# Kernel optimization log

Measured on AMD Instinct MI355X. Metric: run time of the kernel, lower is better.

## Reference

```python
import jax, jax.numpy as jnp
import numpy as np

N = 100_000            # nodes
E = 1_600_000          # edges (avg degree 16)
IN, OUT = 64, 16
L1, L2 = 48, 32        # in - floor(k*(in-out)/3) for k=1,2
EDGE_DIM = 16
EPS = 1e-7             # GENConv message epsilon
BN_EPS = 1e-5


def _lin(k, i, o):
    return jax.random.normal(k, (i, o), jnp.float32) / np.float32(np.sqrt(i))


def setup_inputs() -> dict:
    key = jax.random.key(0)
    ks = jax.random.split(key, 16)
    z = lambda d: jnp.zeros((d,), jnp.float32)
    o = lambda d: jnp.ones((d,), jnp.float32)
    return {
        "x": jax.random.normal(ks[0], (N, IN), jnp.float32),
        "edge_index": jax.random.randint(ks[1], (2, E), 0, N),
        "edge_attr": jax.random.normal(ks[2], (E, EDGE_DIM), jnp.float32),
        # GENConv 1 (IN -> L1)
        "w_src1": _lin(ks[3], IN, L1), "b_src1": z(L1),
        "w_edge1": _lin(ks[4], EDGE_DIM, L1), "b_edge1": z(L1),
        "w_m1a": _lin(ks[5], L1, 2 * L1), "b_m1a": z(2 * L1),
        "g1": o(2 * L1), "be1": z(2 * L1),
        "w_m1b": _lin(ks[6], 2 * L1, L1), "b_m1b": z(L1),
        # GENConv 2 (L1 -> L2)
        "w_src2": _lin(ks[7], L1, L2), "b_src2": z(L2),
        "w_edge2": _lin(ks[8], EDGE_DIM, L2), "b_edge2": z(L2),
        "w_m2a": _lin(ks[9], L2, 2 * L2), "b_m2a": z(2 * L2),
        "g2": o(2 * L2), "be2": z(2 * L2),
        "w_m2b": _lin(ks[10], 2 * L2, L2), "b_m2b": z(L2),
        # GCNConv heads (L2 -> OUT)
        "w_mu": _lin(ks[11], L2, OUT), "b_mu": z(OUT),
        "w_ls": _lin(ks[12], L2, OUT), "b_ls": z(OUT),
    }


def _gen_conv(x, src, dst, e_raw, w_src, b_src, w_edge, b_edge,
              w1, b1, g, be, w2, b2):
    """PyG GENConv with softmax aggregation (t=1) and 2-layer MLP w/ batch norm."""
    h = x @ w_src + b_src                      # [N, d] lin_src
    e = e_raw @ w_edge + b_edge                # [E, d] lin_edge
    msg = jax.nn.relu(h[src] + e) + EPS        # [E, d] message
    # per-destination, per-channel softmax aggregation
    mmax = jax.ops.segment_max(msg, dst, num_segments=N)
    mmax = jnp.where(jnp.isfinite(mmax), mmax, 0.0)
    ex = jnp.exp(msg - mmax[dst])
    denom = jax.ops.segment_sum(ex, dst, num_segments=N)
    agg = jax.ops.segment_sum(ex * msg, dst, num_segments=N) / (denom + 1e-16)
    out = agg + h                              # residual with x_dst (lin_src applied)
    # MLP: Linear -> BatchNorm(train stats) -> ReLU -> Linear
    zt = out @ w1 + b1
    zt = (zt - zt.mean(0)) * jax.lax.rsqrt(zt.var(0) + BN_EPS) * g + be
    return jax.nn.relu(zt) @ w2 + b2


def _gcn_conv(x, src, dst, w, b):
    """PyG GCNConv: self-loops + symmetric normalization."""
    loop = jnp.arange(N)
    s = jnp.concatenate([src, loop])
    d = jnp.concatenate([dst, loop])
    deg = jax.ops.segment_sum(jnp.ones(s.shape, x.dtype), d, num_segments=N)
    dinv = jnp.where(deg > 0, jax.lax.rsqrt(deg), 0.0)
    norm = (dinv[s] * dinv[d])[:, None]
    return jax.ops.segment_sum((x @ w)[s] * norm, d, num_segments=N) + b


def reference(x, edge_index, edge_attr,
              w_src1, b_src1, w_edge1, b_edge1, w_m1a, b_m1a, g1, be1, w_m1b, b_m1b,
              w_src2, b_src2, w_edge2, b_edge2, w_m2a, b_m2a, g2, be2, w_m2b, b_m2b,
              w_mu, b_mu, w_ls, b_ls):
    src, dst = edge_index[0], edge_index[1]
    h = jax.nn.relu(_gen_conv(x, src, dst, edge_attr, w_src1, b_src1, w_edge1,
                              b_edge1, w_m1a, b_m1a, g1, be1, w_m1b, b_m1b))
    h = jax.nn.relu(_gen_conv(h, src, dst, edge_attr, w_src2, b_src2, w_edge2,
                              b_edge2, w_m2a, b_m2a, g2, be2, w_m2b, b_m2b))
    mu = _gcn_conv(h, src, dst, w_mu, b_mu)
    logstd = _gcn_conv(h, src, dst, w_ls, b_ls)
    return (mu, logstd)
```

## Files before the change

kernel.cpp:

```cpp
#include <hip/hip_runtime.h>
#include <hip/hip_bf16.h>

typedef unsigned int u32;

#define EPS_MSG 1e-7f
#define BN_EPS  1e-5f

template<int I, int O>
__global__ void k_lin(const float* __restrict__ X, const float* __restrict__ W,
                      const float* __restrict__ B, float* __restrict__ Y,
                      int ldY, int n) {
  __shared__ float Wl[I * O];
  __shared__ float Bl[O];
  for (int t = threadIdx.x; t < I * O; t += blockDim.x) Wl[t] = W[t];
  if (threadIdx.x < O) Bl[threadIdx.x] = B[threadIdx.x];
  __syncthreads();
  int i = blockIdx.x * blockDim.x + threadIdx.x;
  if (i >= n) return;
  float acc[O];
#pragma unroll
  for (int c = 0; c < O; c++) acc[c] = Bl[c];
  const float4* xp = (const float4*)(X + (size_t)i * I);
  for (int q = 0; q < I / 4; q++) {
    float4 v = xp[q];
#pragma unroll
    for (int c = 0; c < O; c++) acc[c] += v.x * Wl[(4 * q + 0) * O + c];
#pragma unroll
    for (int c = 0; c < O; c++) acc[c] += v.y * Wl[(4 * q + 1) * O + c];
#pragma unroll
    for (int c = 0; c < O; c++) acc[c] += v.z * Wl[(4 * q + 2) * O + c];
#pragma unroll
    for (int c = 0; c < O; c++) acc[c] += v.w * Wl[(4 * q + 3) * O + c];
  }
  float* y = Y + (size_t)i * ldY;
#pragma unroll
  for (int c = 0; c < O; c++) y[c] = acc[c];
}

__global__ void k_deg(const int* __restrict__ ei, u32* __restrict__ deg, int E) {
  int e = blockIdx.x * blockDim.x + threadIdx.x;
  if (e < E) atomicAdd(&deg[ei[E + e]], 1u);
}

__global__ void k_scan1(const u32* __restrict__ deg, u32* __restrict__ excl,
                        u32* __restrict__ part, int n) {
  __shared__ u32 sm[256];
  int t = threadIdx.x;
  int base = blockIdx.x * 1024 + t * 4;
  u32 v0 = (base + 0 < n) ? deg[base + 0] : 0u;
  u32 v1 = (base + 1 < n) ? deg[base + 1] : 0u;
  u32 v2 = (base + 2 < n) ? deg[base + 2] : 0u;
  u32 v3 = (base + 3 < n) ? deg[base + 3] : 0u;
  u32 tsum = v0 + v1 + v2 + v3;
  sm[t] = tsum;
  __syncthreads();
  for (int o = 1; o < 256; o <<= 1) {
    u32 v = (t >= o) ? sm[t - o] : 0u;
    __syncthreads();
    sm[t] += v;
    __syncthreads();
  }
  u32 tex = sm[t] - tsum;
  if (t == 255) part[blockIdx.x] = sm[255];
  if (base + 0 < n) excl[base + 0] = tex;
  if (base + 1 < n) excl[base + 1] = tex + v0;
  if (base + 2 < n) excl[base + 2] = tex + v0 + v1;
  if (base + 3 < n) excl[base + 3] = tex + v0 + v1 + v2;
}

__global__ void k_scan2(u32* __restrict__ part, int nb) {
  if (threadIdx.x == 0) {
    u32 acc = 0;
    for (int i = 0; i < nb; i++) { u32 v = part[i]; part[i] = acc; acc += v; }
  }
}

__global__ void k_scan3(u32* __restrict__ rowptr, const u32* __restrict__ part,
                        int n, int E) {
  int i = blockIdx.x * blockDim.x + threadIdx.x;
  if (i < n) rowptr[i] += part[i >> 10];
  if (i == 0) rowptr[n] = (u32)E;
}

template<bool PERM>
__global__ void k_slots(const int* __restrict__ ei, const u32* __restrict__ rowptr,
                        u32* __restrict__ cnt, int2* __restrict__ csr,
                        const float* __restrict__ ea, float* __restrict__ eaperm,
                        int E) {
  int e = blockIdx.x * blockDim.x + threadIdx.x;
  if (e >= E) return;
  int s = ei[e], d = ei[E + e];
  u32 slot = rowptr[d] + atomicAdd(&cnt[d], 1u);
  csr[slot] = make_int2(s, e);
  if (PERM) {
    const float4* p = (const float4*)(ea + (size_t)e * 16);
    float4* q = (float4*)(eaperm + (size_t)slot * 16);
    float4 a = p[0], b = p[1], c = p[2], dd = p[3];
    q[0] = a; q[1] = b; q[2] = c; q[3] = dd;
  }
}

__global__ void k_dinv(const u32* __restrict__ deg, float* __restrict__ dinv, int n) {
  int i = blockIdx.x * blockDim.x + threadIdx.x;
  if (i < n) dinv[i] = rsqrtf((float)(deg[i] + 1u));
}

template<bool PERM>
__global__ void k_agg48(const u32* __restrict__ rowptr, const int2* __restrict__ csr,
                        const float* __restrict__ attrs,
                        const float* __restrict__ we, const float* __restrict__ be,
                        const float* __restrict__ h, float* __restrict__ out, int n) {
  int lane = threadIdx.x & 63;
  int node = (blockIdx.x * blockDim.x + threadIdx.x) >> 6;
  if (node >= n) return;
  float wc[16];
#pragma unroll
  for (int k = 0; k < 16; k++) wc[k] = 0.f;
  float bias = 0.f;
  if (lane < 48) {
#pragma unroll
    for (int k = 0; k < 16; k++) wc[k] = we[k * 48 + lane];
    bias = be[lane];
  }
  float hself = (lane < 48) ? h[(size_t)node * 48 + lane] : 0.f;
  u32 b = rowptr[node], t = rowptr[node + 1];
  float den = 0.f, num = 0.f;
  u32 i = b;
  if (PERM) {
    if ((i & 1u) && i < t) {
      int2 es = csr[i];
      const float4* p = (const float4*)(attrs + (size_t)i * 16);
      float4 a0 = p[0], a1 = p[1], a2 = p[2], a3 = p[3];
      float hv = (lane < 48) ? h[(size_t)es.x * 48 + lane] : 0.f;
      float ml = bias +
        a0.x * wc[0]  + a0.y * wc[1]  + a0.z * wc[2]  + a0.w * wc[3] +
        a1.x * wc[4]  + a1.y * wc[5]  + a1.z * wc[6]  + a1.w * wc[7] +
        a2.x * wc[8]  + a2.y * wc[9]  + a2.z * wc[10] + a2.w * wc[11] +
        a3.x * wc[12] + a3.y * wc[13] + a3.z * wc[14] + a3.w * wc[15];
      float m = fmaxf(hv + ml, 0.f) + EPS_MSG;
      float ex = __expf(m);
      den += ex; num += ex * m;
      i++;
    }
    for (; i + 2 <= t; i += 2) {
      int4 e01 = *(const int4*)(csr + i);
      const float4* pa = (const float4*)(attrs + (size_t)i * 16);
      float4 a0 = pa[0], a1 = pa[1], a2 = pa[2], a3 = pa[3];
      float4 b0 = pa[4], b1 = pa[5], b2 = pa[6], b3 = pa[7];
      float h0 = (lane < 48) ? h[(size_t)e01.x * 48 + lane] : 0.f;
      float h1 = (lane < 48) ? h[(size_t)e01.z * 48 + lane] : 0.f;
      float ml0 = bias +
        a0.x * wc[0]  + a0.y * wc[1]  + a0.z * wc[2]  + a0.w * wc[3] +
        a1.x * wc[4]  + a1.y * wc[5]  + a1.z * wc[6]  + a1.w * wc[7] +
        a2.x * wc[8]  + a2.y * wc[9]  + a2.z * wc[10] + a2.w * wc[11] +
        a3.x * wc[12] + a3.y * wc[13] + a3.z * wc[14] + a3.w * wc[15];
      float ml1 = bias +
        b0.x * wc[0]  + b0.y * wc[1]  + b0.z * wc[2]  + b0.w * wc[3] +
        b1.x * wc[4]  + b1.y * wc[5]  + b1.z * wc[6]  + b1.w * wc[7] +
        b2.x * wc[8]  + b2.y * wc[9]  + b2.z * wc[10] + b2.w * wc[11] +
        b3.x * wc[12] + b3.y * wc[13] + b3.z * wc[14] + b3.w * wc[15];
      float m0 = fmaxf(h0 + ml0, 0.f) + EPS_MSG;
      float m1 = fmaxf(h1 + ml1, 0.f) + EPS_MSG;
      float ex0 = __expf(m0);
      float ex1 = __expf(m1);
      den += ex0 + ex1;
      num += ex0 * m0 + ex1 * m1;
    }
  }
  for (; i < t; i++) {
    int2 es = csr[i];
    const float4* p = (const float4*)(attrs + (PERM ? (size_t)i : (size_t)es.y) * 16);
    float4 a0 = p[0], a1 = p[1], a2 = p[2], a3 = p[3];
    float hv = (lane < 48) ? h[(size_t)es.x * 48 + lane] : 0.f;
    float ml = bias +
      a0.x * wc[0]  + a0.y * wc[1]  + a0.z * wc[2]  + a0.w * wc[3] +
      a1.x * wc[4]  + a1.y * wc[5]  + a1.z * wc[6]  + a1.w * wc[7] +
      a2.x * wc[8]  + a2.y * wc[9]  + a2.z * wc[10] + a2.w * wc[11] +
      a3.x * wc[12] + a3.y * wc[13] + a3.z * wc[14] + a3.w * wc[15];
    float m = fmaxf(hv + ml, 0.f) + EPS_MSG;
    float ex = __expf(m);
    den += ex; num += ex * m;
  }
  if (lane < 48)
    out[(size_t)node * 48 + lane] = hself + num / (den + 1e-16f);
}

template<bool PERM>
__global__ void k_agg32(const u32* __restrict__ rowptr, const int2* __restrict__ csr,
                        const float* __restrict__ attrs,
                        const float* __restrict__ we, const float* __restrict__ be,
                        const float* __restrict__ h, float* __restrict__ out, int n) {
  int c    = threadIdx.x & 31;
  int node = (blockIdx.x * blockDim.x + threadIdx.x) >> 5;
  if (node >= n) return;
  float wc[16];
#pragma unroll
  for (int k = 0; k < 16; k++) wc[k] = we[k * 32 + c];
  float bias  = be[c];
  float hself = h[(size_t)node * 32 + c];
  u32 b = rowptr[node], t = rowptr[node + 1];
  float den = 0.f, num = 0.f;
  u32 i = b;
  if (PERM) {
    if ((i & 1u) && i < t) {
      int2 es = csr[i];
      const float4* p = (const float4*)(attrs + (size_t)i * 16);
      float4 a0 = p[0], a1 = p[1], a2 = p[2], a3 = p[3];
      float hv = h[(size_t)es.x * 32 + c];
      float ml = bias +
        a0.x * wc[0]  + a0.y * wc[1]  + a0.z * wc[2]  + a0.w * wc[3] +
        a1.x * wc[4]  + a1.y * wc[5]  + a1.z * wc[6]  + a1.w * wc[7] +
        a2.x * wc[8]  + a2.y * wc[9]  + a2.z * wc[10] + a2.w * wc[11] +
        a3.x * wc[12] + a3.y * wc[13] + a3.z * wc[14] + a3.w * wc[15];
      float m = fmaxf(hv + ml, 0.f) + EPS_MSG;
      float ex = __expf(m);
      den += ex; num += ex * m;
      i++;
    }
    for (; i + 2 <= t; i += 2) {
      int4 e01 = *(const int4*)(csr + i);
      const float4* pa = (const float4*)(attrs + (size_t)i * 16);
      float4 a0 = pa[0], a1 = pa[1], a2 = pa[2], a3 = pa[3];
      float4 b0 = pa[4], b1 = pa[5], b2 = pa[6], b3 = pa[7];
      float h0 = h[(size_t)e01.x * 32 + c];
      float h1 = h[(size_t)e01.z * 32 + c];
      float ml0 = bias +
        a0.x * wc[0]  + a0.y * wc[1]  + a0.z * wc[2]  + a0.w * wc[3] +
        a1.x * wc[4]  + a1.y * wc[5]  + a1.z * wc[6]  + a1.w * wc[7] +
        a2.x * wc[8]  + a2.y * wc[9]  + a2.z * wc[10] + a2.w * wc[11] +
        a3.x * wc[12] + a3.y * wc[13] + a3.z * wc[14] + a3.w * wc[15];
      float ml1 = bias +
        b0.x * wc[0]  + b0.y * wc[1]  + b0.z * wc[2]  + b0.w * wc[3] +
        b1.x * wc[4]  + b1.y * wc[5]  + b1.z * wc[6]  + b1.w * wc[7] +
        b2.x * wc[8]  + b2.y * wc[9]  + b2.z * wc[10] + b2.w * wc[11] +
        b3.x * wc[12] + b3.y * wc[13] + b3.z * wc[14] + b3.w * wc[15];
      float m0 = fmaxf(h0 + ml0, 0.f) + EPS_MSG;
      float m1 = fmaxf(h1 + ml1, 0.f) + EPS_MSG;
      float ex0 = __expf(m0);
      float ex1 = __expf(m1);
      den += ex0 + ex1;
      num += ex0 * m0 + ex1 * m1;
    }
  }
  for (; i < t; i++) {
    int2 es = csr[i];
    const float4* p = (const float4*)(attrs + (PERM ? (size_t)i : (size_t)es.y) * 16);
    float4 a0 = p[0], a1 = p[1], a2 = p[2], a3 = p[3];
    float hv = h[(size_t)es.x * 32 + c];
    float ml = bias +
      a0.x * wc[0]  + a0.y * wc[1]  + a0.z * wc[2]  + a0.w * wc[3] +
      a1.x * wc[4]  + a1.y * wc[5]  + a1.z * wc[6]  + a1.w * wc[7] +
      a2.x * wc[8]  + a2.y * wc[9]  + a2.z * wc[10] + a2.w * wc[11] +
      a3.x * wc[12] + a3.y * wc[13] + a3.z * wc[14] + a3.w * wc[15];
    float m = fmaxf(hv + ml, 0.f) + EPS_MSG;
    float ex = __expf(m);
    den += ex; num += ex * m;
  }
  out[(size_t)node * 32 + c] = hself + num / (den + 1e-16f);
}

template<int D>
__global__ void k_ztstats(const float* __restrict__ X, const float* __restrict__ W,
                          const float* __restrict__ B, float* __restrict__ Z1,
                          float* __restrict__ Z2, float* __restrict__ partial, int n) {
  __shared__ float Wl[D * 2 * D];
  __shared__ float Bl[2 * D];
  __shared__ float red[4][4 * D];
  for (int t = threadIdx.x; t < D * 2 * D; t += blockDim.x) Wl[t] = W[t];
  for (int t = threadIdx.x; t < 2 * D; t += blockDim.x) Bl[t] = B[t];
  __syncthreads();
  int i = blockIdx.x * blockDim.x + threadIdx.x;
  bool act = (i < n);
  float acc[2 * D];
#pragma unroll
  for (int c = 0; c < 2 * D; c++) acc[c] = 0.f;
  if (act) {
#pragma unroll
    for (int c = 0; c < 2 * D; c++) acc[c] = Bl[c];
    const float4* xp = (const float4*)(X + (size_t)i * D);
    for (int q = 0; q < D / 4; q++) {
      float4 v = xp[q];
#pragma unroll
      for (int c = 0; c < 2 * D; c++) acc[c] += v.x * Wl[(4 * q + 0) * 2 * D + c];
#pragma unroll
      for (int c = 0; c < 2 * D; c++) acc[c] += v.y * Wl[(4 * q + 1) * 2 * D + c];
#pragma unroll
      for (int c = 0; c < 2 * D; c++) acc[c] += v.z * Wl[(4 * q + 2) * 2 * D + c];
#pragma unroll
      for (int c = 0; c < 2 * D; c++) acc[c] += v.w * Wl[(4 * q + 3) * 2 * D + c];
    }
    float* z1 = Z1 + (size_t)i * D;
    float* z2 = Z2 + (size_t)i * D;
#pragma unroll
    for (int c = 0; c < D; c++) { z1[c] = acc[c]; z2[c] = acc[D + c]; }
  } else {
#pragma unroll
    for (int c = 0; c < 2 * D; c++) acc[c] = 0.f;
  }
  int lane = threadIdx.x & 63;
  int wv   = threadIdx.x >> 6;
#pragma unroll
  for (int c = 0; c < 2 * D; c++) {
    float v = acc[c], v2 = v * v;
#pragma unroll
    for (int o = 32; o; o >>= 1) { v += __shfl_xor(v, o); v2 += __shfl_xor(v2, o); }
    if (lane == 0) { red[wv][c] = v; red[wv][2 * D + c] = v2; }
  }
  __syncthreads();
  if (threadIdx.x < 4 * D) {
    float s = red[0][threadIdx.x] + red[1][threadIdx.x] +
              red[2][threadIdx.x] + red[3][threadIdx.x];
    partial[(size_t)blockIdx.x * 4 * D + threadIdx.x] = s;
  }
}

__global__ void k_bnfin(const float* __restrict__ partial, float* __restrict__ stats,
                        int nb, int m) {
  int c = blockIdx.x * blockDim.x + threadIdx.x;
  if (c >= m) return;
  float s = 0.f;
  for (int b = 0; b < nb; b++) s += partial[(size_t)b * m + c];
  stats[c] = s;
}

template<int D, int DD, int O, bool ADDBS>
__global__ void k_mlp_lin(const float* __restrict__ ztA, const float* __restrict__ ztB,
                          const float* __restrict__ stats,
                          const float* __restrict__ G, const float* __restrict__ BE,
                          const float* __restrict__ W2, const float* __restrict__ B2,
                          const float* __restrict__ Wsa, const float* __restrict__ Wsb,
                          const float* __restrict__ Bs,
                          float* __restrict__ out, float invN, int n) {
  __shared__ float Wl[DD * D];
  __shared__ float Ws[D * O];
  __shared__ float Bl[D];
  __shared__ float Bsl[O];
  __shared__ float sc[DD], sh[DD];
  for (int t = threadIdx.x; t < DD * D; t += blockDim.x) Wl[t] = W2[t];
  if (Wsb == nullptr) {
    for (int t = threadIdx.x; t < D * O; t += blockDim.x) Ws[t] = Wsa[t];
  } else {
    for (int t = threadIdx.x; t < D * O; t += blockDim.x) {
      int k = t / O, o = t % O;
      Ws[t] = (o < O / 2) ? Wsa[k * (O / 2) + o] : Wsb[k * (O / 2) + (o - O / 2)];
    }
  }
  if (threadIdx.x < D) Bl[threadIdx.x] = B2[threadIdx.x];
  if (threadIdx.x < O) Bsl[threadIdx.x] = ADDBS ? Bs[threadIdx.x] : 0.f;
  if (threadIdx.x < DD) {
    int c   = threadIdx.x;
    float m = stats[c] * invN;
    float v = stats[DD + c] * invN - m * m;
    float s = G[c] * rsqrtf(v + BN_EPS);
    sc[c] = s; sh[c] = BE[c] - m * s;
  }
  __syncthreads();
  int i = blockIdx.x * blockDim.x + threadIdx.x;
  if (i >= n) return;
  float y[D];
#pragma unroll
  for (int c = 0; c < D; c++) y[c] = Bl[c];
  const float* a = ztA + (size_t)i * D;
  const float* b = ztB + (size_t)i * D;
  for (int k = 0; k < D; k++) {
    float z = fmaxf(a[k] * sc[k] + sh[k], 0.f);
#pragma unroll
    for (int c = 0; c < D; c++) y[c] += z * Wl[k * D + c];
  }
  for (int k = D; k < DD; k++) {
    float z = fmaxf(b[k - D] * sc[k] + sh[k], 0.f);
#pragma unroll
    for (int c = 0; c < D; c++) y[c] += z * Wl[k * D + c];
  }
  float acc[O];
#pragma unroll
  for (int o = 0; o < O; o++) acc[o] = Bsl[o];
#pragma unroll
  for (int k = 0; k < D; k++) {
    float z = fmaxf(y[k], 0.f);
#pragma unroll
    for (int o = 0; o < O; o++) acc[o] += z * Ws[k * O + o];
  }
  float* yo = out + (size_t)i * O;
#pragma unroll
  for (int o = 0; o < O; o++) yo[o] = acc[o];
}

__global__ void k_gcn(const u32* __restrict__ rowptr, const int2* __restrict__ csr,
                      const float* __restrict__ yz, const float* __restrict__ dinv,
                      const float* __restrict__ bmu, const float* __restrict__ bls,
                      float* __restrict__ out, int n) {
  int c    = threadIdx.x & 31;
  int node = (blockIdx.x * blockDim.x + threadIdx.x) >> 5;
  if (node >= n) return;
  u32 b = rowptr[node], t = rowptr[node + 1];
  float acc = 0.f;
  u32 i = b;
  for (; i + 2 <= t; i += 2) {
    int s0 = csr[i].x;
    int s1 = csr[i + 1].x;
    float y0 = yz[(size_t)s0 * 32 + c];
    float y1 = yz[(size_t)s1 * 32 + c];
    float d0 = dinv[s0];
    float d1 = dinv[s1];
    acc += y0 * d0 + y1 * d1;
  }
  if (i < t) {
    int s0 = csr[i].x;
    acc += yz[(size_t)s0 * 32 + c] * dinv[s0];
  }
  float dv  = dinv[node];
  float val = (acc + yz[(size_t)node * 32 + c] * dv) * dv +
              ((c < 16) ? bmu[c] : bls[c - 16]);
  if (c < 16) out[(size_t)node * 16 + c] = val;
  else        out[(size_t)n * 16 + (size_t)node * 16 + (c - 16)] = val;
}

extern "C" void kernel_launch(void* const* d_in, const int* in_sizes, int n_in,
                              void* d_out, int out_size, void* d_ws, size_t ws_size,
                              hipStream_t stream) {
  const float* x      = (const float*)d_in[0];
  const int*  ei      = (const int*)d_in[1];
  const float* ea     = (const float*)d_in[2];
  const float* w_src1 = (const float*)d_in[3];  const float* b_src1 = (const float*)d_in[4];
  const float* w_edge1= (const float*)d_in[5];  const float* b_edge1= (const float*)d_in[6];
  const float* w_m1a  = (const float*)d_in[7];  const float* b_m1a  = (const float*)d_in[8];
  const float* g1     = (const float*)d_in[9];  const float* be1    = (const float*)d_in[10];
  const float* w_m1b  = (const float*)d_in[11]; const float* b_m1b  = (const float*)d_in[12];
  const float* w_src2 = (const float*)d_in[13]; const float* b_src2 = (const float*)d_in[14];
  const float* w_edge2= (const float*)d_in[15]; const float* b_edge2= (const float*)d_in[16];
  const float* w_m2a  = (const float*)d_in[17]; const float* b_m2a  = (const float*)d_in[18];
  const float* g2     = (const float*)d_in[19]; const float* be2    = (const float*)d_in[20];
  const float* w_m2b  = (const float*)d_in[21]; const float* b_m2b  = (const float*)d_in[22];
  const float* w_mu   = (const float*)d_in[23]; const float* b_mu   = (const float*)d_in[24];
  const float* w_ls   = (const float*)d_in[25]; const float* b_ls   = (const float*)d_in[26];

  const int N = in_sizes[0] / 64;
  const int E = in_sizes[1] / 2;

  const int NB  = (N + 255) / 256;
  const int EB  = (E + 255) / 256;
  const int SB1 = (N + 1023) / 1024;

  float* ws     = (float*)d_ws;
  size_t N48    = (size_t)N * 48;
  float* P0     = ws;
  float* P1     = ws + N48;
  float* P2     = ws + 2 * N48;
  float* P3     = ws + 3 * N48;
  size_t o      = 4 * N48;
  u32*  rowptr  = (u32*)(ws + o);
  u32*  cnt     = rowptr + (N + 1);
  u32*  deg     = cnt + N;
  u32*  part    = deg + N;
  float* dinv   = (float*)(part + 256);
  float* stats  = dinv + N;
  size_t po     = o + 4 * (size_t)N + 769;
  float* partial= ws + po;
  size_t co     = (po + (size_t)NB * 192 + 3) & ~(size_t)3;
  int2* csr     = (int2*)(ws + co);
  size_t eo     = co + 2 * (size_t)E;
  float* eaperm = ws + eo;
  size_t needB  = (eo + 16 * (size_t)E + 16) * sizeof(float);
  const bool PERM = (ws_size >= needB);

  dim3 b256(256);

  hipMemsetAsync(cnt, 0, 2 * (size_t)N * sizeof(u32), stream);

  k_deg<<<EB, b256, 0, stream>>>(ei, deg, E);
  k_scan1<<<SB1, b256, 0, stream>>>(deg, rowptr, part, N);
  k_scan2<<<1, 64, 0, stream>>>(part, SB1);
  k_scan3<<<NB, b256, 0, stream>>>(rowptr, part, N, E);
  if (PERM) k_slots<true><<<EB, b256, 0, stream>>>(ei, rowptr, cnt, csr, ea, eaperm, E);
  else      k_slots<false><<<EB, b256, 0, stream>>>(ei, rowptr, cnt, csr, ea, eaperm, E);
  k_dinv<<<NB, b256, 0, stream>>>(deg, dinv, N);

  const float* attrs = PERM ? eaperm : ea;

  k_lin<64, 48><<<NB, b256, 0, stream>>>(x, w_src1, b_src1, P0, 48, N);
  if (PERM) k_agg48<true><<<(N * 64 + 255) / 256, b256, 0, stream>>>(rowptr, csr, attrs,
                                                     w_edge1, b_edge1, P0, P3, N);
  else      k_agg48<false><<<(N * 64 + 255) / 256, b256, 0, stream>>>(rowptr, csr, attrs,
                                                     w_edge1, b_edge1, P0, P3, N);
  k_ztstats<48><<<NB, b256, 0, stream>>>(P3, w_m1a, b_m1a, P1, P2, partial, N);
  k_bnfin<<<1, 256, 0, stream>>>(partial, stats, NB, 192);
  k_mlp_lin<48, 96, 32, true><<<NB, b256, 0, stream>>>(P1, P2, stats, g1, be1,
                                                       w_m1b, b_m1b, w_src2, nullptr,
                                                       b_src2, P0, 1.0f / (float)N, N);

  if (PERM) k_agg32<true><<<(N * 32 + 255) / 256, b256, 0, stream>>>(rowptr, csr, attrs,
                                                     w_edge2, b_edge2, P0, P3, N);
  else      k_agg32<false><<<(N * 32 + 255) / 256, b256, 0, stream>>>(rowptr, csr, attrs,
                                                     w_edge2, b_edge2, P0, P3, N);
  k_ztstats<32><<<NB, b256, 0, stream>>>(P3, w_m2a, b_m2a, P1, P2, partial, N);
  k_bnfin<<<1, 256, 0, stream>>>(partial, stats + 256, NB, 128);
  k_mlp_lin<32, 64, 32, false><<<NB, b256, 0, stream>>>(P1, P2, stats + 256, g2, be2,
                                                        w_m2b, b_m2b, w_mu, w_ls,
                                                        nullptr, P0, 1.0f / (float)N, N);

  k_gcn<<<(N * 32 + 255) / 256, b256, 0, stream>>>(rowptr, csr, P0, dinv,
                                                   b_mu, b_ls, (float*)d_out, N);
}
```

Measured before the change: 1.091 ms.

## Split CSR into separate src/eid arrays and gather edge attrs in separate pass

Replaces the interleaved int2 CSR (src, edge id) with two separate int arrays. The aggregation and GCN kernels then read only the source indices they need, halving index traffic. The edge-attribute permutation moves out of the atomic slot kernel into its own gather kernel, which reads scattered rows and writes them contiguously instead of scattering writes. The cost is one extra kernel launch and a second pass that re-reads the edge-id array.

```diff
diff --git a/kernel.cpp b/kernel.cpp
--- a/kernel.cpp
+++ b/kernel.cpp
@@ -82,22 +82,26 @@
   if (i == 0) rowptr[n] = (u32)E;
 }
 
-template<bool PERM>
 __global__ void k_slots(const int* __restrict__ ei, const u32* __restrict__ rowptr,
-                        u32* __restrict__ cnt, int2* __restrict__ csr,
-                        const float* __restrict__ ea, float* __restrict__ eaperm,
-                        int E) {
+                        u32* __restrict__ cnt, int* __restrict__ csr_src,
+                        int* __restrict__ csr_eid, int E) {
   int e = blockIdx.x * blockDim.x + threadIdx.x;
   if (e >= E) return;
   int s = ei[e], d = ei[E + e];
   u32 slot = rowptr[d] + atomicAdd(&cnt[d], 1u);
-  csr[slot] = make_int2(s, e);
-  if (PERM) {
-    const float4* p = (const float4*)(ea + (size_t)e * 16);
-    float4* q = (float4*)(eaperm + (size_t)slot * 16);
-    float4 a = p[0], b = p[1], c = p[2], dd = p[3];
-    q[0] = a; q[1] = b; q[2] = c; q[3] = dd;
-  }
+  csr_src[slot] = s;
+  csr_eid[slot] = e;
+}
+
+__global__ void k_gather(const int* __restrict__ csr_eid, const float* __restrict__ ea,
+                         float* __restrict__ eaperm, int E) {
+  int i = blockIdx.x * blockDim.x + threadIdx.x;
+  if (i >= E) return;
+  int e = csr_eid[i];
+  const float4* p = (const float4*)(ea + (size_t)e * 16);
+  float4* q = (float4*)(eaperm + (size_t)i * 16);
+  float4 a = p[0], b = p[1], c = p[2], d = p[3];
+  q[0] = a; q[1] = b; q[2] = c; q[3] = d;
 }
 
 __global__ void k_dinv(const u32* __restrict__ deg, float* __restrict__ dinv, int n) {
@@ -106,8 +110,8 @@
 }
 
 template<bool PERM>
-__global__ void k_agg48(const u32* __restrict__ rowptr, const int2* __restrict__ csr,
-                        const float* __restrict__ attrs,
+__global__ void k_agg48(const u32* __restrict__ rowptr, const int* __restrict__ csr_src,
+                        const int* __restrict__ csr_eid, const float* __restrict__ attrs,
                         const float* __restrict__ we, const float* __restrict__ be,
                         const float* __restrict__ h, float* __restrict__ out, int n) {
   int lane = threadIdx.x & 63;
@@ -128,10 +132,10 @@
   u32 i = b;
   if (PERM) {
     if ((i & 1u) && i < t) {
-      int2 es = csr[i];
+      int s = csr_src[i];
       const float4* p = (const float4*)(attrs + (size_t)i * 16);
       float4 a0 = p[0], a1 = p[1], a2 = p[2], a3 = p[3];
-      float hv = (lane < 48) ? h[(size_t)es.x * 48 + lane] : 0.f;
+      float hv = (lane < 48) ? h[(size_t)s * 48 + lane] : 0.f;
       float ml = bias +
         a0.x * wc[0]  + a0.y * wc[1]  + a0.z * wc[2]  + a0.w * wc[3] +
         a1.x * wc[4]  + a1.y * wc[5]  + a1.z * wc[6]  + a1.w * wc[7] +
@@ -143,12 +147,12 @@
       i++;
     }
     for (; i + 2 <= t; i += 2) {
-      int4 e01 = *(const int4*)(csr + i);
+      int2 ss = *(const int2*)(csr_src + i);
       const float4* pa = (const float4*)(attrs + (size_t)i * 16);
       float4 a0 = pa[0], a1 = pa[1], a2 = pa[2], a3 = pa[3];
       float4 b0 = pa[4], b1 = pa[5], b2 = pa[6], b3 = pa[7];
-      float h0 = (lane < 48) ? h[(size_t)e01.x * 48 + lane] : 0.f;
-      float h1 = (lane < 48) ? h[(size_t)e01.z * 48 + lane] : 0.f;
+      float h0 = (lane < 48) ? h[(size_t)ss.x * 48 + lane] : 0.f;
+      float h1 = (lane < 48) ? h[(size_t)ss.y * 48 + lane] : 0.f;
       float ml0 = bias +
         a0.x * wc[0]  + a0.y * wc[1]  + a0.z * wc[2]  + a0.w * wc[3] +
         a1.x * wc[4]  + a1.y * wc[5]  + a1.z * wc[6]  + a1.w * wc[7] +
@@ -168,10 +172,10 @@
     }
   }
   for (; i < t; i++) {
-    int2 es = csr[i];
-    const float4* p = (const float4*)(attrs + (PERM ? (size_t)i : (size_t)es.y) * 16);
+    int s = csr_src[i];
+    const float4* p = (const float4*)(attrs + (PERM ? (size_t)i : (size_t)csr_eid[i]) * 16);
     float4 a0 = p[0], a1 = p[1], a2 = p[2], a3 = p[3];
-    float hv = (lane < 48) ? h[(size_t)es.x * 48 + lane] : 0.f;
+    float hv = (lane < 48) ? h[(size_t)s * 48 + lane] : 0.f;
     float ml = bias +
       a0.x * wc[0]  + a0.y * wc[1]  + a0.z * wc[2]  + a0.w * wc[3] +
       a1.x * wc[4]  + a1.y * wc[5]  + a1.z * wc[6]  + a1.w * wc[7] +
@@ -186,8 +190,8 @@
 }
 
 template<bool PERM>
-__global__ void k_agg32(const u32* __restrict__ rowptr, const int2* __restrict__ csr,
-                        const float* __restrict__ attrs,
+__global__ void k_agg32(const u32* __restrict__ rowptr, const int* __restrict__ csr_src,
+                        const int* __restrict__ csr_eid, const float* __restrict__ attrs,
                         const float* __restrict__ we, const float* __restrict__ be,
                         const float* __restrict__ h, float* __restrict__ out, int n) {
   int c    = threadIdx.x & 31;
@@ -203,10 +207,10 @@
   u32 i = b;
   if (PERM) {
     if ((i & 1u) && i < t) {
-      int2 es = csr[i];
+      int s = csr_src[i];
       const float4* p = (const float4*)(attrs + (size_t)i * 16);
       float4 a0 = p[0], a1 = p[1], a2 = p[2], a3 = p[3];
-      float hv = h[(size_t)es.x * 32 + c];
+      float hv = h[(size_t)s * 32 + c];
       float ml = bias +
         a0.x * wc[0]  + a0.y * wc[1]  + a0.z * wc[2]  + a0.w * wc[3] +
         a1.x * wc[4]  + a1.y * wc[5]  + a1.z * wc[6]  + a1.w * wc[7] +
@@ -218,12 +222,12 @@
       i++;
     }
     for (; i + 2 <= t; i += 2) {
-      int4 e01 = *(const int4*)(csr + i);
+      int2 ss = *(const int2*)(csr_src + i);
       const float4* pa = (const float4*)(attrs + (size_t)i * 16);
       float4 a0 = pa[0], a1 = pa[1], a2 = pa[2], a3 = pa[3];
       float4 b0 = pa[4], b1 = pa[5], b2 = pa[6], b3 = pa[7];
-      float h0 = h[(size_t)e01.x * 32 + c];
-      float h1 = h[(size_t)e01.z * 32 + c];
+      float h0 = h[(size_t)ss.x * 32 + c];
+      float h1 = h[(size_t)ss.y * 32 + c];
       float ml0 = bias +
         a0.x * wc[0]  + a0.y * wc[1]  + a0.z * wc[2]  + a0.w * wc[3] +
         a1.x * wc[4]  + a1.y * wc[5]  + a1.z * wc[6]  + a1.w * wc[7] +
@@ -243,10 +247,10 @@
     }
   }
   for (; i < t; i++) {
-    int2 es = csr[i];
-    const float4* p = (const float4*)(attrs + (PERM ? (size_t)i : (size_t)es.y) * 16);
+    int s = csr_src[i];
+    const float4* p = (const float4*)(attrs + (PERM ? (size_t)i : (size_t)csr_eid[i]) * 16);
     float4 a0 = p[0], a1 = p[1], a2 = p[2], a3 = p[3];
-    float hv = h[(size_t)es.x * 32 + c];
+    float hv = h[(size_t)s * 32 + c];
     float ml = bias +
       a0.x * wc[0]  + a0.y * wc[1]  + a0.z * wc[2]  + a0.w * wc[3] +
       a1.x * wc[4]  + a1.y * wc[5]  + a1.z * wc[6]  + a1.w * wc[7] +
@@ -386,7 +390,7 @@
   for (int o = 0; o < O; o++) yo[o] = acc[o];
 }
 
-__global__ void k_gcn(const u32* __restrict__ rowptr, const int2* __restrict__ csr,
+__global__ void k_gcn(const u32* __restrict__ rowptr, const int* __restrict__ csr_src,
                       const float* __restrict__ yz, const float* __restrict__ dinv,
                       const float* __restrict__ bmu, const float* __restrict__ bls,
                       float* __restrict__ out, int n) {
@@ -397,8 +401,8 @@
   float acc = 0.f;
   u32 i = b;
   for (; i + 2 <= t; i += 2) {
-    int s0 = csr[i].x;
-    int s1 = csr[i + 1].x;
+    int s0 = csr_src[i];
+    int s1 = csr_src[i + 1];
     float y0 = yz[(size_t)s0 * 32 + c];
     float y1 = yz[(size_t)s1 * 32 + c];
     float d0 = dinv[s0];
@@ -406,7 +410,7 @@
     acc += y0 * d0 + y1 * d1;
   }
   if (i < t) {
-    int s0 = csr[i].x;
+    int s0 = csr_src[i];
     acc += yz[(size_t)s0 * 32 + c] * dinv[s0];
   }
   float dv  = dinv[node];
@@ -458,7 +462,8 @@
   size_t po     = o + 4 * (size_t)N + 769;
   float* partial= ws + po;
   size_t co     = (po + (size_t)NB * 192 + 3) & ~(size_t)3;
-  int2* csr     = (int2*)(ws + co);
+  int*  csr_src = (int*)(ws + co);
+  int*  csr_eid = csr_src + E;
   size_t eo     = co + 2 * (size_t)E;
   float* eaperm = ws + eo;
   size_t needB  = (eo + 16 * (size_t)E + 16) * sizeof(float);
@@ -472,33 +477,33 @@
   k_scan1<<<SB1, b256, 0, stream>>>(deg, rowptr, part, N);
   k_scan2<<<1, 64, 0, stream>>>(part, SB1);
   k_scan3<<<NB, b256, 0, stream>>>(rowptr, part, N, E);
-  if (PERM) k_slots<true><<<EB, b256, 0, stream>>>(ei, rowptr, cnt, csr, ea, eaperm, E);
-  else      k_slots<false><<<EB, b256, 0, stream>>>(ei, rowptr, cnt, csr, ea, eaperm, E);
+  k_slots<<<EB, b256, 0, stream>>>(ei, rowptr, cnt, csr_src, csr_eid, E);
+  if (PERM) k_gather<<<EB, b256, 0, stream>>>(csr_eid, ea, eaperm, E);
   k_dinv<<<NB, b256, 0, stream>>>(deg, dinv, N);
 
   const float* attrs = PERM ? eaperm : ea;
 
   k_lin<64, 48><<<NB, b256, 0, stream>>>(x, w_src1, b_src1, P0, 48, N);
-  if (PERM) k_agg48<true><<<(N * 64 + 255) / 256, b256, 0, stream>>>(rowptr, csr, attrs,
-                                                     w_edge1, b_edge1, P0, P3, N);
-  else      k_agg48<false><<<(N * 64 + 255) / 256, b256, 0, stream>>>(rowptr, csr, attrs,
-                                                     w_edge1, b_edge1, P0, P3, N);
+  if (PERM) k_agg48<true><<<(N * 64 + 255) / 256, b256, 0, stream>>>(rowptr, csr_src,
+                                           csr_eid, attrs, w_edge1, b_edge1, P0, P3, N);
+  else      k_agg48<false><<<(N * 64 + 255) / 256, b256, 0, stream>>>(rowptr, csr_src,
+                                           csr_eid, attrs, w_edge1, b_edge1, P0, P3, N);
   k_ztstats<48><<<NB, b256, 0, stream>>>(P3, w_m1a, b_m1a, P1, P2, partial, N);
   k_bnfin<<<1, 256, 0, stream>>>(partial, stats, NB, 192);
   k_mlp_lin<48, 96, 32, true><<<NB, b256, 0, stream>>>(P1, P2, stats, g1, be1,
                                                        w_m1b, b_m1b, w_src2, nullptr,
                                                        b_src2, P0, 1.0f / (float)N, N);
 
-  if (PERM) k_agg32<true><<<(N * 32 + 255) / 256, b256, 0, stream>>>(rowptr, csr, attrs,
-                                                     w_edge2, b_edge2, P0, P3, N);
-  else      k_agg32<false><<<(N * 32 + 255) / 256, b256, 0, stream>>>(rowptr, csr, attrs,
-                                                     w_edge2, b_edge2, P0, P3, N);
+  if (PERM) k_agg32<true><<<(N * 32 + 255) / 256, b256, 0, stream>>>(rowptr, csr_src,
+                                           csr_eid, attrs, w_edge2, b_edge2, P0, P3, N);
+  else      k_agg32<false><<<(N * 32 + 255) / 256, b256, 0, stream>>>(rowptr, csr_src,
+                                           csr_eid, attrs, w_edge2, b_edge2, P0, P3, N);
   k_ztstats<32><<<NB, b256, 0, stream>>>(P3, w_m2a, b_m2a, P1, P2, partial, N);
   k_bnfin<<<1, 256, 0, stream>>>(partial, stats + 256, NB, 128);
   k_mlp_lin<32, 64, 32, false><<<NB, b256, 0, stream>>>(P1, P2, stats + 256, g2, be2,
                                                         w_m2b, b_m2b, w_mu, w_ls,
                                                         nullptr, P0, 1.0f / (float)N, N);
 
-  k_gcn<<<(N * 32 + 255) / 256, b256, 0, stream>>>(rowptr, csr, P0, dinv,
+  k_gcn<<<(N * 32 + 255) / 256, b256, 0, stream>>>(rowptr, csr_src, P0, dinv,
                                                    b_mu, b_ls, (float*)d_out, N);
 }
```

Measured after the change: 1.100 ms. No clear change (+0.9%).
